# Kernel tuning notes

Measured on AMD Instinct MI355X. Metric: run time of the kernel, lower is better.

The kernel has to match this reference:

```python
import jax, jax.numpy as jnp
import numpy as np

NEG_SLOPE = 0.2
EPS = 1e-16

N_NODES = 50000
N_EDGES = 800000
IN_C = 256
HID_C = 64
HEADS = 4
OUT_C = 128
N_GRAPHS = 100


def setup_inputs() -> dict:
    key = jax.random.key(0)
    ks = jax.random.split(key, 12)
    x = jax.random.normal(ks[0], (N_NODES, IN_C), dtype=jnp.float32)
    edge_index = jax.random.randint(ks[1], (2, N_EDGES), 0, N_NODES, dtype=jnp.int64)
    batch = jnp.sort(jax.random.randint(ks[2], (N_NODES,), 0, N_GRAPHS, dtype=jnp.int64))
    s1 = 1.0 / np.sqrt(IN_C)
    s2 = 1.0 / np.sqrt(HEADS * HID_C)
    W1 = jax.random.uniform(ks[3], (IN_C, HEADS * HID_C), jnp.float32, -s1, s1)
    att_src1 = jax.random.uniform(ks[4], (HEADS, HID_C), jnp.float32, -s1, s1)
    att_dst1 = jax.random.uniform(ks[5], (HEADS, HID_C), jnp.float32, -s1, s1)
    bias1 = jnp.zeros((HEADS * HID_C,), jnp.float32)
    W2 = jax.random.uniform(ks[6], (HEADS * HID_C, OUT_C), jnp.float32, -s2, s2)
    att_src2 = jax.random.uniform(ks[7], (1, OUT_C), jnp.float32, -s2, s2)
    att_dst2 = jax.random.uniform(ks[8], (1, OUT_C), jnp.float32, -s2, s2)
    bias2 = jnp.zeros((OUT_C,), jnp.float32)
    return {"x": x, "W1": W1, "att_src1": att_src1, "att_dst1": att_dst1,
            "bias1": bias1, "W2": W2, "att_src2": att_src2, "att_dst2": att_dst2,
            "bias2": bias2, "edge_index": edge_index, "batch": batch,
            "num_graphs": N_GRAPHS}


def gat_conv(x, W, att_src, att_dst, bias, src, dst, heads, ch):
    # x: [N, F_in]; W: [F_in, heads*ch]; att_*: [heads, ch]
    n = x.shape[0]
    h = (x @ W).reshape(n, heads, ch)                      # [N, H, C]
    a_src = jnp.sum(h * att_src[None], axis=-1)            # [N, H]
    a_dst = jnp.sum(h * att_dst[None], axis=-1)            # [N, H]
    alpha = a_src[src] + a_dst[dst]                        # [E, H]
    alpha = jax.nn.leaky_relu(alpha, NEG_SLOPE)
    # segment softmax over destination nodes (every node has a self-loop)
    amax = jax.ops.segment_max(alpha, dst, num_segments=n)
    e = jnp.exp(alpha - amax[dst])
    denom = jax.ops.segment_sum(e, dst, num_segments=n)
    alpha = e / (denom[dst] + EPS)                         # [E, H]
    msg = h[src] * alpha[:, :, None]                       # [E, H, C]
    out = jax.ops.segment_sum(msg, dst, num_segments=n)    # [N, H, C]
    return out.reshape(n, heads * ch) + bias


def reference(x, W1, att_src1, att_dst1, bias1, W2, att_src2, att_dst2, bias2,
              edge_index, batch, num_graphs):
    n = x.shape[0]
    loops = jnp.arange(n, dtype=edge_index.dtype)
    src = jnp.concatenate([edge_index[0], loops])
    dst = jnp.concatenate([edge_index[1], loops])
    h = gat_conv(x, W1, att_src1, att_dst1, bias1, src, dst, HEADS, HID_C)
    h = jax.nn.relu(h)
    h = gat_conv(h, W2, att_src2, att_dst2, bias2, src, dst, 1, OUT_C)
    h = jax.nn.relu(h)
    # global mean pool over graphs
    sums = jax.ops.segment_sum(h, batch, num_segments=num_graphs)
    cnt = jax.ops.segment_sum(jnp.ones((n, 1), h.dtype), batch, num_segments=num_graphs)
    return sums / jnp.maximum(cnt, 1.0)
```

## Files before the change

kernel.cpp:

```cpp
#include <hip/hip_runtime.h>
#include <hip/hip_bf16.h>
#include <hip/hip_fp16.h>

#define N_NODES 50000
#define N_EDGES 800000
#define E_TOT   (N_EDGES + N_NODES)
#define IN_C    256
#define H1C     256
#define HEADS   4
#define HID_C   64
#define OUT_C   128
#define N_GRAPHS 100
#define NEG_SLOPE 0.2f
#define EPS_F 1e-16f

#define NBUCKET 391
#define BIN_BLOCKS 104
#define EDGES_PER_SB 8192
#define EBUF_CAP 4096
#define STAGE_CAP 4096
#define GEMM1_MB 391

#define PREP_BIN_BLOCKS    104
#define PREP_CAST_BLOCKS   12500
#define PREP_W1_BLOCKS     256
#define PREP_W2_BLOCKS     128
#define PREP_BOUNDS_BLOCKS 196
#define PREP_DOUT_BLOCKS   50
#define PREP_TOTAL (PREP_BIN_BLOCKS + PREP_CAST_BLOCKS + PREP_W1_BLOCKS + PREP_W2_BLOCKS + PREP_BOUNDS_BLOCKS + PREP_DOUT_BLOCKS)

typedef _Float16 half8_t __attribute__((ext_vector_type(8)));
typedef float f32x4 __attribute__((ext_vector_type(4)));

__device__ __forceinline__ void gll16(const void* g, void* l) {
    __builtin_amdgcn_global_load_lds(
        (const __attribute__((address_space(1))) void*)g,
        (__attribute__((address_space(3))) void*)l, 16, 0, 0);
}

__global__ __launch_bounds__(256) void prep_kernel(const float* __restrict__ x,
                                                   _Float16* __restrict__ xh,
                                                   const float* __restrict__ W1,
                                                   _Float16* __restrict__ W1t,
                                                   const float* __restrict__ W2,
                                                   _Float16* __restrict__ W2t,
                                                   const int* __restrict__ ei,
                                                   int* __restrict__ gcur,
                                                   int* __restrict__ ebuf,
                                                   const int* __restrict__ batch,
                                                   int* __restrict__ gstart,
                                                   float* __restrict__ d_out) {
    __shared__ int bh[NBUCKET];
    __shared__ int bofs[NBUCKET];
    int b = blockIdx.x;
    int tid = threadIdx.x;
    if (b < PREP_BIN_BLOCKS) {
        for (int t = tid; t < NBUCKET; t += 256) bh[t] = 0;
        __syncthreads();
        int base = b * EDGES_PER_SB;
#pragma unroll 4
        for (int k = 0; k < EDGES_PER_SB / 256; ++k) {
            int idx = base + k * 256 + tid;
            int d = -1;
            if (idx < N_EDGES) d = ei[N_EDGES + idx];
            else if (idx < E_TOT) d = idx - N_EDGES;
            if (d >= 0 && d < N_NODES) atomicAdd(&bh[d >> 7], 1);
        }
        __syncthreads();
        for (int t = tid; t < NBUCKET; t += 256) {
            int c = bh[t];
            bofs[t] = (c > 0) ? atomicAdd(&gcur[t], c) : 0;
            bh[t] = 0;
        }
        __syncthreads();
#pragma unroll 4
        for (int k = 0; k < EDGES_PER_SB / 256; ++k) {
            int idx = base + k * 256 + tid;
            int s = 0, d = -1;
            if (idx < N_EDGES) { s = ei[idx]; d = ei[N_EDGES + idx]; }
            else if (idx < E_TOT) { s = idx - N_EDGES; d = s; }
            if (d >= 0 && d < N_NODES) {
                int t = d >> 7;
                int p = bofs[t] + atomicAdd(&bh[t], 1);
                if (p < EBUF_CAP)
                    ebuf[t * EBUF_CAP + p] = (s & 0xFFFF) | ((d & 127) << 16);
            }
        }
        return;
    }
    b -= PREP_BIN_BLOCKS;
    if (b < PREP_CAST_BLOCKS) {
        int idx = b * 256 + tid;
        float4 v = reinterpret_cast<const float4*>(x)[idx];
        union { _Float16 h[4]; uint2 u; } p;
        p.h[0] = (_Float16)v.x; p.h[1] = (_Float16)v.y;
        p.h[2] = (_Float16)v.z; p.h[3] = (_Float16)v.w;
        reinterpret_cast<uint2*>(xh)[idx] = p.u;
        return;
    }
    b -= PREP_CAST_BLOCKS;
    if (b < PREP_W1_BLOCKS) {
        int idx = b * 256 + tid;
        int n = idx >> 8, k = idx & 255;
        W1t[idx] = (_Float16)W1[k * 256 + n];
        return;
    }
    b -= PREP_W1_BLOCKS;
    if (b < PREP_W2_BLOCKS) {
        int idx = b * 256 + tid;
        int n = idx >> 8, k = idx & 255;
        W2t[idx] = (_Float16)W2[k * 128 + n];
        return;
    }
    b -= PREP_W2_BLOCKS;
    if (b < PREP_BOUNDS_BLOCKS) {
        int idx = b * 256 + tid;
        if (idx >= N_NODES) return;
        int g = batch[idx];
        if (g < 0) g = 0; if (g >= N_GRAPHS) g = N_GRAPHS - 1;
        if (idx == 0) {
            for (int j = 0; j <= g; ++j) gstart[j] = 0;
        } else {
            int gp = batch[idx - 1];
            if (gp < 0) gp = 0; if (gp >= N_GRAPHS) gp = N_GRAPHS - 1;
            for (int j = gp + 1; j <= g; ++j) gstart[j] = idx;
        }
        if (idx == N_NODES - 1) {
            for (int j = g + 1; j <= N_GRAPHS; ++j) gstart[j] = N_NODES;
        }
        return;
    }
    b -= PREP_BOUNDS_BLOCKS;
    {
        int idx = b * 256 + tid;
        if (idx < N_GRAPHS * 128) d_out[idx] = 0.f;
    }
}

__global__ __launch_bounds__(256) void sort_gemm1_kernel(const int* __restrict__ gcur,
                                                         const int* __restrict__ ebuf,
                                                         int* __restrict__ ssrc,
                                                         int* __restrict__ row_ptr,
                                                         const _Float16* __restrict__ A,
                                                         const _Float16* __restrict__ Bt,
                                                         _Float16* __restrict__ C,
                                                         const float* __restrict__ attS,
                                                         const float* __restrict__ attD,
                                                         float* __restrict__ a_src_o,
                                                         float* __restrict__ a_dst_o) {
    __shared__ __align__(16) char smem[17408];
    __shared__ int s_off;
    const int tid = threadIdx.x;

    if (blockIdx.x < NBUCKET) {
        int* cnt   = reinterpret_cast<int*>(smem);
        int* sc    = cnt + 128;
        int* stage = sc + 128;
        int j = blockIdx.x;
        if (tid < 64) {
            int acc = 0;
            for (int i = tid; i < j; i += 64) {
                int c = gcur[i];
                acc += (c < EBUF_CAP) ? c : EBUF_CAP;
            }
#pragma unroll
            for (int off = 32; off > 0; off >>= 1) acc += __shfl_down(acc, off);
            if (tid == 0) s_off = acc;
        }
        if (tid < 128) cnt[tid] = 0;
        __syncthreads();
        int span = gcur[j]; if (span > EBUF_CAP) span = EBUF_CAP;
        int lo = s_off;
        const int* eb = ebuf + j * EBUF_CAP;
        for (int t = tid; t < span; t += 256)
            atomicAdd(&cnt[(eb[t] >> 16) & 127], 1);
        __syncthreads();
        if (tid < 128) sc[tid] = cnt[tid];
        __syncthreads();
#pragma unroll
        for (int off = 1; off < 128; off <<= 1) {
            int u = (tid >= off && tid < 128) ? sc[tid - off] : 0;
            __syncthreads();
            if (tid < 128) sc[tid] += u;
            __syncthreads();
        }
        int jn0 = j << 7;
        int nNodes = N_NODES - jn0; if (nNodes > 128) nNodes = 128;
        if (tid < 128) {
            int excl = sc[tid] - cnt[tid];
            if (tid < nNodes) row_ptr[jn0 + tid] = lo + excl;
            cnt[tid] = excl;
        }
        if (j == NBUCKET - 1 && tid == 0) row_ptr[N_NODES] = lo + span;
        __syncthreads();
        for (int t = tid; t < span; t += 256) {
            int v = eb[t];
            int p = atomicAdd(&cnt[(v >> 16) & 127], 1);
            stage[p] = v & 0xFFFF;
        }
        __syncthreads();
        for (int t = tid; t < span; t += 256) ssrc[lo + t] = stage[t];
        return;
    }

    _Float16* As = reinterpret_cast<_Float16*>(smem);
    _Float16* Bs = reinterpret_cast<_Float16*>(smem + 8192);
    int b2 = blockIdx.x - NBUCKET;
    const int tileM = (b2 >= GEMM1_MB ? b2 - GEMM1_MB : b2) * 128;
    const int tileN = (b2 >= GEMM1_MB) ? 128 : 0;
    const int w = tid >> 6, lane = tid & 63;
    const int wm = (w >> 1) * 64, wn = (w & 1) * 64;
    const int quad = lane >> 4, mlane = lane & 15;
    const int lrow = lane >> 2;
    const int pos  = lane & 3;
    const int ra0  = w * 16 + lrow;
    const int ra1  = ra0 + 64;
    const int ca0  = pos ^ ((ra0 >> 1) & 3);
    const int ca1  = pos ^ ((ra1 >> 1) & 3);

    f32x4 zero = {0.f, 0.f, 0.f, 0.f};
    f32x4 acc[4][4];
#pragma unroll
    for (int i = 0; i < 4; ++i)
#pragma unroll
        for (int j = 0; j < 4; ++j) acc[i][j] = zero;

    const _Float16* gA0 = A + (size_t)(tileM + ra0) * 256 + ca0 * 8;
    const _Float16* gA1 = A + (size_t)(tileM + ra1) * 256 + ca1 * 8;
    const _Float16* gB0 = Bt + (size_t)(tileN + ra0) * 256 + ca0 * 8;
    const _Float16* gB1 = Bt + (size_t)(tileN + ra1) * 256 + ca1 * 8;
    _Float16* lA0 = As + w * 512;
    _Float16* lA1 = As + 2048 + w * 512;
    _Float16* lB0 = Bs + w * 512;
    _Float16* lB1 = Bs + 2048 + w * 512;

    for (int k0 = 0; k0 < 256; k0 += 32) {
        __syncthreads();
        gll16(gA0 + k0, lA0);
        gll16(gA1 + k0, lA1);
        gll16(gB0 + k0, lB0);
        gll16(gB1 + k0, lB1);
        __syncthreads();
        half8_t af[4], bf[4];
#pragma unroll
        for (int mt = 0; mt < 4; ++mt) {
            int ra = wm + mt * 16 + mlane;
            af[mt] = *reinterpret_cast<const half8_t*>(As + ra * 32 + ((quad ^ ((ra >> 1) & 3)) << 3));
        }
#pragma unroll
        for (int nt = 0; nt < 4; ++nt) {
            int rb = wn + nt * 16 + mlane;
            bf[nt] = *reinterpret_cast<const half8_t*>(Bs + rb * 32 + ((quad ^ ((rb >> 1) & 3)) << 3));
        }
#pragma unroll
        for (int mt = 0; mt < 4; ++mt)
#pragma unroll
            for (int nt = 0; nt < 4; ++nt)
                acc[mt][nt] = __builtin_amdgcn_mfma_f32_16x16x32_f16(af[mt], bf[nt], acc[mt][nt], 0, 0, 0);
    }
#pragma unroll
    for (int mt = 0; mt < 4; ++mt) {
#pragma unroll
        for (int i = 0; i < 4; ++i) {
            int row = tileM + wm + mt * 16 + quad * 4 + i;
            if (row < N_NODES) {
                _Float16* cp = C + (size_t)row * 256 + tileN + wn;
#pragma unroll
                for (int nt = 0; nt < 4; ++nt)
                    cp[nt * 16 + mlane] = (_Float16)acc[mt][nt][i];
            }
        }
    }
    {
        int hd = (tileN + wn) >> 6;
        float as[4], ad[4];
#pragma unroll
        for (int nt = 0; nt < 4; ++nt) {
            as[nt] = attS[hd * 64 + nt * 16 + mlane];
            ad[nt] = attD[hd * 64 + nt * 16 + mlane];
        }
#pragma unroll
        for (int mt = 0; mt < 4; ++mt) {
#pragma unroll
            for (int i = 0; i < 4; ++i) {
                float ps = acc[mt][0][i] * as[0] + acc[mt][1][i] * as[1]
                         + acc[mt][2][i] * as[2] + acc[mt][3][i] * as[3];
                float pd = acc[mt][0][i] * ad[0] + acc[mt][1][i] * ad[1]
                         + acc[mt][2][i] * ad[2] + acc[mt][3][i] * ad[3];
#pragma unroll
                for (int off = 1; off < 16; off <<= 1) {
                    ps += __shfl_xor(ps, off);
                    pd += __shfl_xor(pd, off);
                }
                if (mlane == 0) {
                    int row = tileM + wm + mt * 16 + quad * 4 + i;
                    if (row < N_NODES) {
                        a_src_o[row * 4 + hd] = ps;
                        a_dst_o[row * 4 + hd] = pd;
                    }
                }
            }
        }
    }
}

__global__ __launch_bounds__(256) void gemm_mfma_kernel(const _Float16* __restrict__ A,
                                                        const _Float16* __restrict__ Bt,
                                                        _Float16* __restrict__ C,
                                                        const float* __restrict__ attS,
                                                        const float* __restrict__ attD,
                                                        float* __restrict__ a_src_o,
                                                        float* __restrict__ a_dst_o,
                                                        int M, int N) {
    __shared__ __align__(16) _Float16 As[4096];
    __shared__ __align__(16) _Float16 Bs[4096];
    __shared__ float lds_ps[128];
    __shared__ float lds_pd[128];
    const int tid = threadIdx.x;
    const int tileM = blockIdx.x * 128;
    const int tileN = 0;
    const int w = tid >> 6, lane = tid & 63;
    const int wm = (w >> 1) * 64, wn = (w & 1) * 64;
    const int quad = lane >> 4, mlane = lane & 15;
    const int lrow = lane >> 2;
    const int pos  = lane & 3;
    const int ra0  = w * 16 + lrow;
    const int ra1  = ra0 + 64;
    const int ca0  = pos ^ ((ra0 >> 1) & 3);
    const int ca1  = pos ^ ((ra1 >> 1) & 3);

    f32x4 zero = {0.f, 0.f, 0.f, 0.f};
    f32x4 acc[4][4];
#pragma unroll
    for (int i = 0; i < 4; ++i)
#pragma unroll
        for (int j = 0; j < 4; ++j) acc[i][j] = zero;

    const _Float16* gA0 = A + (size_t)(tileM + ra0) * 256 + ca0 * 8;
    const _Float16* gA1 = A + (size_t)(tileM + ra1) * 256 + ca1 * 8;
    const _Float16* gB0 = Bt + (size_t)(tileN + ra0) * 256 + ca0 * 8;
    const _Float16* gB1 = Bt + (size_t)(tileN + ra1) * 256 + ca1 * 8;
    _Float16* lA0 = As + w * 512;
    _Float16* lA1 = As + 2048 + w * 512;
    _Float16* lB0 = Bs + w * 512;
    _Float16* lB1 = Bs + 2048 + w * 512;

    for (int k0 = 0; k0 < 256; k0 += 32) {
        __syncthreads();
        gll16(gA0 + k0, lA0);
        gll16(gA1 + k0, lA1);
        gll16(gB0 + k0, lB0);
        gll16(gB1 + k0, lB1);
        __syncthreads();
        half8_t af[4], bf[4];
#pragma unroll
        for (int mt = 0; mt < 4; ++mt) {
            int ra = wm + mt * 16 + mlane;
            af[mt] = *reinterpret_cast<const half8_t*>(As + ra * 32 + ((quad ^ ((ra >> 1) & 3)) << 3));
        }
#pragma unroll
        for (int nt = 0; nt < 4; ++nt) {
            int rb = wn + nt * 16 + mlane;
            bf[nt] = *reinterpret_cast<const half8_t*>(Bs + rb * 32 + ((quad ^ ((rb >> 1) & 3)) << 3));
        }
#pragma unroll
        for (int mt = 0; mt < 4; ++mt)
#pragma unroll
            for (int nt = 0; nt < 4; ++nt)
                acc[mt][nt] = __builtin_amdgcn_mfma_f32_16x16x32_f16(af[mt], bf[nt], acc[mt][nt], 0, 0, 0);
    }
#pragma unroll
    for (int mt = 0; mt < 4; ++mt) {
#pragma unroll
        for (int i = 0; i < 4; ++i) {
            int row = tileM + wm + mt * 16 + quad * 4 + i;
            if (row < M) {
                _Float16* cp = C + (size_t)row * N + tileN + wn;
#pragma unroll
                for (int nt = 0; nt < 4; ++nt)
                    cp[nt * 16 + mlane] = (_Float16)acc[mt][nt][i];
            }
        }
    }
    {
        float as[4], ad[4];
#pragma unroll
        for (int nt = 0; nt < 4; ++nt) {
            as[nt] = attS[wn + nt * 16 + mlane];
            ad[nt] = attD[wn + nt * 16 + mlane];
        }
        float psa[4][4], pda[4][4];
#pragma unroll
        for (int mt = 0; mt < 4; ++mt) {
#pragma unroll
            for (int i = 0; i < 4; ++i) {
                float ps = acc[mt][0][i] * as[0] + acc[mt][1][i] * as[1]
                         + acc[mt][2][i] * as[2] + acc[mt][3][i] * as[3];
                float pd = acc[mt][0][i] * ad[0] + acc[mt][1][i] * ad[1]
                         + acc[mt][2][i] * ad[2] + acc[mt][3][i] * ad[3];
#pragma unroll
                for (int off = 1; off < 16; off <<= 1) {
                    ps += __shfl_xor(ps, off);
                    pd += __shfl_xor(pd, off);
                }
                psa[mt][i] = ps; pda[mt][i] = pd;
            }
        }
        __syncthreads();
        if (wn == 0 && mlane == 0) {
#pragma unroll
            for (int mt = 0; mt < 4; ++mt)
#pragma unroll
                for (int i = 0; i < 4; ++i) {
                    int lr = wm + mt * 16 + quad * 4 + i;
                    lds_ps[lr] = psa[mt][i];
                    lds_pd[lr] = pda[mt][i];
                }
        }
        __syncthreads();
        if (wn == 64 && mlane == 0) {
#pragma unroll
            for (int mt = 0; mt < 4; ++mt)
#pragma unroll
                for (int i = 0; i < 4; ++i) {
                    int lr = wm + mt * 16 + quad * 4 + i;
                    int row = tileM + lr;
                    if (row < M) {
                        a_src_o[row] = psa[mt][i] + lds_ps[lr];
                        a_dst_o[row] = pda[mt][i] + lds_pd[lr];
                    }
                }
        }
    }
}

__device__ __forceinline__ float lrelu(float x) { return x > 0.f ? x : NEG_SLOPE * x; }

__global__ __launch_bounds__(256) void edge1_kernel(const int* __restrict__ row_ptr,
                                                    const int* __restrict__ ssrc,
                                                    const __half* __restrict__ h1h,
                                                    const float* __restrict__ a_src,
                                                    const float* __restrict__ a_dst,
                                                    const float* __restrict__ bias,
                                                    __half* __restrict__ out) {
    int node = blockIdx.x * 4 + (threadIdx.x >> 6);
    int lane = threadIdx.x & 63;
    int hf   = lane >> 5;
    int cl   = lane & 31;
    int hd   = cl >> 3;
    int start = row_ptr[node], end = row_ptr[node + 1];
    int em1 = end - 1;
    float adh = a_dst[node * 4 + hd];

    const uint4* h1v = reinterpret_cast<const uint4*>(h1h);
    float4 aA0 = make_float4(0.f,0.f,0.f,0.f), aA1 = make_float4(0.f,0.f,0.f,0.f);
    float4 aB0 = make_float4(0.f,0.f,0.f,0.f), aB1 = make_float4(0.f,0.f,0.f,0.f);
    float s = 0.f;
    for (int e = start; e < end; e += 4) {
        int e0 = e + hf;
        int e1 = e + 2 + hf;
        int i0 = ssrc[e0 <= em1 ? e0 : em1];
        int i1 = ssrc[e1 <= em1 ? e1 : em1];
        float r0 = a_src[i0 * 4 + hd];
        float r1 = a_src[i1 * 4 + hd];
        uint4 q0 = h1v[(size_t)i0 * 32 + cl];
        uint4 q1 = h1v[(size_t)i1 * 32 + cl];
        float w0 = (e0 < end) ? __expf(lrelu(r0 + adh)) : 0.f;
        float w1 = (e1 < end) ? __expf(lrelu(r1 + adh)) : 0.f;
        s += w0 + w1;
        float2 f;
        f = __half22float2(*reinterpret_cast<const __half2*>(&q0.x)); aA0.x += w0*f.x; aA0.y += w0*f.y;
        f = __half22float2(*reinterpret_cast<const __half2*>(&q0.y)); aA0.z += w0*f.x; aA0.w += w0*f.y;
        f = __half22float2(*reinterpret_cast<const __half2*>(&q0.z)); aA1.x += w0*f.x; aA1.y += w0*f.y;
        f = __half22float2(*reinterpret_cast<const __half2*>(&q0.w)); aA1.z += w0*f.x; aA1.w += w0*f.y;
        f = __half22float2(*reinterpret_cast<const __half2*>(&q1.x)); aB0.x += w1*f.x; aB0.y += w1*f.y;
        f = __half22float2(*reinterpret_cast<const __half2*>(&q1.y)); aB0.z += w1*f.x; aB0.w += w1*f.y;
        f = __half22float2(*reinterpret_cast<const __half2*>(&q1.z)); aB1.x += w1*f.x; aB1.y += w1*f.y;
        f = __half22float2(*reinterpret_cast<const __half2*>(&q1.w)); aB1.z += w1*f.x; aB1.w += w1*f.y;
    }
    float4 c0, c1;
    c0.x = aA0.x + aB0.x; c0.y = aA0.y + aB0.y; c0.z = aA0.z + aB0.z; c0.w = aA0.w + aB0.w;
    c1.x = aA1.x + aB1.x; c1.y = aA1.y + aB1.y; c1.z = aA1.z + aB1.z; c1.w = aA1.w + aB1.w;
    c0.x += __shfl_xor(c0.x, 32); c0.y += __shfl_xor(c0.y, 32);
    c0.z += __shfl_xor(c0.z, 32); c0.w += __shfl_xor(c0.w, 32);
    c1.x += __shfl_xor(c1.x, 32); c1.y += __shfl_xor(c1.y, 32);
    c1.z += __shfl_xor(c1.z, 32); c1.w += __shfl_xor(c1.w, 32);
    s += __shfl_xor(s, 32);
    float inv = 1.0f / (s + EPS_F);
    if (lane < 32) {
        const float4* b4 = reinterpret_cast<const float4*>(bias);
        float4 b0 = b4[cl * 2], b1 = b4[cl * 2 + 1];
        union { _Float16 h[8]; uint4 u; } st;
        st.h[0] = (_Float16)fmaxf(c0.x * inv + b0.x, 0.f);
        st.h[1] = (_Float16)fmaxf(c0.y * inv + b0.y, 0.f);
        st.h[2] = (_Float16)fmaxf(c0.z * inv + b0.z, 0.f);
        st.h[3] = (_Float16)fmaxf(c0.w * inv + b0.w, 0.f);
        st.h[4] = (_Float16)fmaxf(c1.x * inv + b1.x, 0.f);
        st.h[5] = (_Float16)fmaxf(c1.y * inv + b1.y, 0.f);
        st.h[6] = (_Float16)fmaxf(c1.z * inv + b1.z, 0.f);
        st.h[7] = (_Float16)fmaxf(c1.w * inv + b1.w, 0.f);
        reinterpret_cast<uint4*>(out)[(size_t)node * 32 + cl] = st.u;
    }
}

__global__ __launch_bounds__(256) void edge2_kernel(const int* __restrict__ row_ptr,
                                                    const int* __restrict__ ssrc,
                                                    const __half* __restrict__ h2h,
                                                    const float* __restrict__ a_src,
                                                    const float* __restrict__ a_dst,
                                                    const float* __restrict__ bias,
                                                    float* __restrict__ out) {
    int lane = threadIdx.x & 63;
    int node = blockIdx.x * 8 + ((threadIdx.x >> 6) << 1) + (lane >> 5);
    int sub  = (lane >> 4) & 1;
    int cl   = lane & 15;
    int start = row_ptr[node], end = row_ptr[node + 1];
    int em1 = end - 1;
    float ad = a_dst[node];

    const uint4* h2v = reinterpret_cast<const uint4*>(h2h);
    float4 aA0 = make_float4(0.f,0.f,0.f,0.f), aA1 = make_float4(0.f,0.f,0.f,0.f);
    float4 aB0 = make_float4(0.f,0.f,0.f,0.f), aB1 = make_float4(0.f,0.f,0.f,0.f);
    float s = 0.f;
    for (int e = start; e < end; e += 4) {
        int e0 = e + sub;
        int e1 = e + 2 + sub;
        int i0 = ssrc[e0 <= em1 ? e0 : em1];
        int i1 = ssrc[e1 <= em1 ? e1 : em1];
        float r0 = a_src[i0];
        float r1 = a_src[i1];
        uint4 q0 = h2v[(size_t)i0 * 16 + cl];
        uint4 q1 = h2v[(size_t)i1 * 16 + cl];
        float w0 = (e0 < end) ? __expf(lrelu(r0 + ad)) : 0.f;
        float w1 = (e1 < end) ? __expf(lrelu(r1 + ad)) : 0.f;
        s += w0 + w1;
        float2 f;
        f = __half22float2(*reinterpret_cast<const __half2*>(&q0.x)); aA0.x += w0*f.x; aA0.y += w0*f.y;
        f = __half22float2(*reinterpret_cast<const __half2*>(&q0.y)); aA0.z += w0*f.x; aA0.w += w0*f.y;
        f = __half22float2(*reinterpret_cast<const __half2*>(&q0.z)); aA1.x += w0*f.x; aA1.y += w0*f.y;
        f = __half22float2(*reinterpret_cast<const __half2*>(&q0.w)); aA1.z += w0*f.x; aA1.w += w0*f.y;
        f = __half22float2(*reinterpret_cast<const __half2*>(&q1.x)); aB0.x += w1*f.x; aB0.y += w1*f.y;
        f = __half22float2(*reinterpret_cast<const __half2*>(&q1.y)); aB0.z += w1*f.x; aB0.w += w1*f.y;
        f = __half22float2(*reinterpret_cast<const __half2*>(&q1.z)); aB1.x += w1*f.x; aB1.y += w1*f.y;
        f = __half22float2(*reinterpret_cast<const __half2*>(&q1.w)); aB1.z += w1*f.x; aB1.w += w1*f.y;
    }
    float4 c0, c1;
    c0.x = aA0.x + aB0.x; c0.y = aA0.y + aB0.y; c0.z = aA0.z + aB0.z; c0.w = aA0.w + aB0.w;
    c1.x = aA1.x + aB1.x; c1.y = aA1.y + aB1.y; c1.z = aA1.z + aB1.z; c1.w = aA1.w + aB1.w;
    c0.x += __shfl_xor(c0.x, 16); c0.y += __shfl_xor(c0.y, 16);
    c0.z += __shfl_xor(c0.z, 16); c0.w += __shfl_xor(c0.w, 16);
    c1.x += __shfl_xor(c1.x, 16); c1.y += __shfl_xor(c1.y, 16);
    c1.z += __shfl_xor(c1.z, 16); c1.w += __shfl_xor(c1.w, 16);
    s += __shfl_xor(s, 16);
    float inv = 1.0f / (s + EPS_F);
    if (sub == 0) {
        const float4* b4 = reinterpret_cast<const float4*>(bias);
        float4 b0 = b4[cl * 2], b1 = b4[cl * 2 + 1];
        float4 o0, o1;
        o0.x = fmaxf(c0.x * inv + b0.x, 0.f);
        o0.y = fmaxf(c0.y * inv + b0.y, 0.f);
        o0.z = fmaxf(c0.z * inv + b0.z, 0.f);
        o0.w = fmaxf(c0.w * inv + b0.w, 0.f);
        o1.x = fmaxf(c1.x * inv + b1.x, 0.f);
        o1.y = fmaxf(c1.y * inv + b1.y, 0.f);
        o1.z = fmaxf(c1.z * inv + b1.z, 0.f);
        o1.w = fmaxf(c1.w * inv + b1.w, 0.f);
        float4* o4 = reinterpret_cast<float4*>(out) + (size_t)node * 32 + cl * 2;
        o4[0] = o0;
        o4[1] = o1;
    }
}

#define POOL_CHUNK 64
__global__ __launch_bounds__(128) void pool_kernel(const float* __restrict__ out2,
                                                   const int* __restrict__ batch,
                                                   const int* __restrict__ gstart,
                                                   float* __restrict__ d_out) {
    int c = threadIdx.x;
    int node0 = blockIdx.x * POOL_CHUNK;
    int nodeEnd = node0 + POOL_CHUNK; if (nodeEnd > N_NODES) nodeEnd = N_NODES;
    if (node0 >= N_NODES) return;
    int gprev = batch[node0];
    float acc = 0.f;
    for (int node = node0; node < nodeEnd; ++node) {
        int g = batch[node];
        if (g != gprev) {
            if (gprev >= 0 && gprev < N_GRAPHS) {
                float cnt = (float)(gstart[gprev + 1] - gstart[gprev]);
                if (cnt < 1.f) cnt = 1.f;
                atomicAdd(&d_out[gprev * 128 + c], acc / cnt);
            }
            acc = 0.f;
            gprev = g;
        }
        acc += out2[(size_t)node * 128 + c];
    }
    if (gprev >= 0 && gprev < N_GRAPHS) {
        float cnt = (float)(gstart[gprev + 1] - gstart[gprev]);
        if (cnt < 1.f) cnt = 1.f;
        atomicAdd(&d_out[gprev * 128 + c], acc / cnt);
    }
}

extern "C" void kernel_launch(void* const* d_in, const int* in_sizes, int n_in,
                              void* d_out_v, int out_size, void* d_ws, size_t ws_size,
                              hipStream_t stream) {
    const float* x      = (const float*)d_in[0];
    const float* W1     = (const float*)d_in[1];
    const float* att_s1 = (const float*)d_in[2];
    const float* att_d1 = (const float*)d_in[3];
    const float* bias1  = (const float*)d_in[4];
    const float* W2     = (const float*)d_in[5];
    const float* att_s2 = (const float*)d_in[6];
    const float* att_d2 = (const float*)d_in[7];
    const float* bias2  = (const float*)d_in[8];
    const int*   ei     = (const int*)d_in[9];
    const int*   batch  = (const int*)d_in[10];
    float* d_out = (float*)d_out_v;

    float* ws = (float*)d_ws;
    _Float16* xh    = (_Float16*)ws;
    _Float16* h1h   = (_Float16*)(ws + 6400000);
    _Float16* out1h = (_Float16*)(ws + 12800000);
    _Float16* h2h   = (_Float16*)ws;
    float*    out2  = ws + 6400000;
    float* a_src1 = ws + 19200000;
    float* a_dst1 = a_src1 + 200000;
    float* a_src2 = a_dst1 + 200000;
    float* a_dst2 = a_src2 + 50000;
    int* row_ptr  = (int*)(a_dst2 + 50000);
    int* ssrc     = row_ptr + 50016;
    int* ebuf     = ssrc + 850000;
    int* gcur     = ebuf + (NBUCKET * EBUF_CAP);
    int* gstart   = gcur + 512;
    _Float16* W1t = (_Float16*)(gstart + 128);
    _Float16* W2t = W1t + 65536;

    hipMemsetAsync(gcur, 0, 512 * sizeof(int), stream);

    prep_kernel<<<PREP_TOTAL, 256, 0, stream>>>(x, xh, W1, W1t, W2, W2t,
                                                ei, gcur, ebuf,
                                                batch, gstart, d_out);

    sort_gemm1_kernel<<<NBUCKET + GEMM1_MB * 2, 256, 0, stream>>>(
        gcur, ebuf, ssrc, row_ptr, xh, W1t, h1h,
        att_s1, att_d1, a_src1, a_dst1);

    edge1_kernel<<<N_NODES / 4, 256, 0, stream>>>(row_ptr, ssrc, (const __half*)h1h,
                                                  a_src1, a_dst1, bias1, (__half*)out1h);

    gemm_mfma_kernel<<<(N_NODES + 127) / 128, 256, 0, stream>>>(
        out1h, W2t, h2h, att_s2, att_d2, a_src2, a_dst2, N_NODES, OUT_C);

    edge2_kernel<<<N_NODES / 8, 256, 0, stream>>>(row_ptr, ssrc, (const __half*)h2h,
                                                  a_src2, a_dst2, bias2, out2);

    pool_kernel<<<(N_NODES + POOL_CHUNK - 1) / POOL_CHUNK, 128, 0, stream>>>(out2, batch, gstart, d_out);
}
```

Before: 293.3 us.

## Fuse fp32-to-fp16 cast of x into GEMM1 with full-width N tiles

Drops the separate prep pass that converts x to fp16 in a workspace buffer. GEMM1 now reads fp32 x directly, converts it in registers and writes it into shared memory. Each block is widened to 512 threads and covers all 256 output columns, so each A row is loaded once instead of twice. This removes a 51MB read plus 25MB write pass, at the cost of synchronous global loads for A instead of async LDS loads and larger blocks for the sort path.

```diff
diff --git a/kernel.cpp b/kernel.cpp
--- a/kernel.cpp
+++ b/kernel.cpp
@@ -15,19 +15,17 @@
 #define EPS_F 1e-16f
 
 #define NBUCKET 391
-#define BIN_BLOCKS 104
 #define EDGES_PER_SB 8192
 #define EBUF_CAP 4096
 #define STAGE_CAP 4096
 #define GEMM1_MB 391
 
 #define PREP_BIN_BLOCKS    104
-#define PREP_CAST_BLOCKS   12500
 #define PREP_W1_BLOCKS     256
 #define PREP_W2_BLOCKS     128
 #define PREP_BOUNDS_BLOCKS 196
 #define PREP_DOUT_BLOCKS   50
-#define PREP_TOTAL (PREP_BIN_BLOCKS + PREP_CAST_BLOCKS + PREP_W1_BLOCKS + PREP_W2_BLOCKS + PREP_BOUNDS_BLOCKS + PREP_DOUT_BLOCKS)
+#define PREP_TOTAL (PREP_BIN_BLOCKS + PREP_W1_BLOCKS + PREP_W2_BLOCKS + PREP_BOUNDS_BLOCKS + PREP_DOUT_BLOCKS)
 
 typedef _Float16 half8_t __attribute__((ext_vector_type(8)));
 typedef float f32x4 __attribute__((ext_vector_type(4)));
@@ -38,9 +36,7 @@
         (__attribute__((address_space(3))) void*)l, 16, 0, 0);
 }
 
-__global__ __launch_bounds__(256) void prep_kernel(const float* __restrict__ x,
-                                                   _Float16* __restrict__ xh,
-                                                   const float* __restrict__ W1,
+__global__ __launch_bounds__(256) void prep_kernel(const float* __restrict__ W1,
                                                    _Float16* __restrict__ W1t,
                                                    const float* __restrict__ W2,
                                                    _Float16* __restrict__ W2t,
@@ -89,16 +85,6 @@
         return;
     }
     b -= PREP_BIN_BLOCKS;
-    if (b < PREP_CAST_BLOCKS) {
-        int idx = b * 256 + tid;
-        float4 v = reinterpret_cast<const float4*>(x)[idx];
-        union { _Float16 h[4]; uint2 u; } p;
-        p.h[0] = (_Float16)v.x; p.h[1] = (_Float16)v.y;
-        p.h[2] = (_Float16)v.z; p.h[3] = (_Float16)v.w;
-        reinterpret_cast<uint2*>(xh)[idx] = p.u;
-        return;
-    }
-    b -= PREP_CAST_BLOCKS;
     if (b < PREP_W1_BLOCKS) {
         int idx = b * 256 + tid;
         int n = idx >> 8, k = idx & 255;
@@ -137,18 +123,18 @@
     }
 }
 
-__global__ __launch_bounds__(256) void sort_gemm1_kernel(const int* __restrict__ gcur,
+__global__ __launch_bounds__(512) void sort_gemm1_kernel(const int* __restrict__ gcur,
                                                          const int* __restrict__ ebuf,
                                                          int* __restrict__ ssrc,
                                                          int* __restrict__ row_ptr,
-                                                         const _Float16* __restrict__ A,
+                                                         const float* __restrict__ X,
                                                          const _Float16* __restrict__ Bt,
                                                          _Float16* __restrict__ C,
                                                          const float* __restrict__ attS,
                                                          const float* __restrict__ attD,
                                                          float* __restrict__ a_src_o,
                                                          float* __restrict__ a_dst_o) {
-    __shared__ __align__(16) char smem[17408];
+    __shared__ __align__(16) char smem[24576];
     __shared__ int s_off;
     const int tid = threadIdx.x;
 
@@ -172,7 +158,7 @@
         int span = gcur[j]; if (span > EBUF_CAP) span = EBUF_CAP;
         int lo = s_off;
         const int* eb = ebuf + j * EBUF_CAP;
-        for (int t = tid; t < span; t += 256)
+        for (int t = tid; t < span; t += 512)
             atomicAdd(&cnt[(eb[t] >> 16) & 127], 1);
         __syncthreads();
         if (tid < 128) sc[tid] = cnt[tid];
@@ -193,30 +179,34 @@
         }
         if (j == NBUCKET - 1 && tid == 0) row_ptr[N_NODES] = lo + span;
         __syncthreads();
-        for (int t = tid; t < span; t += 256) {
+        for (int t = tid; t < span; t += 512) {
             int v = eb[t];
             int p = atomicAdd(&cnt[(v >> 16) & 127], 1);
             stage[p] = v & 0xFFFF;
         }
         __syncthreads();
-        for (int t = tid; t < span; t += 256) ssrc[lo + t] = stage[t];
+        for (int t = tid; t < span; t += 512) ssrc[lo + t] = stage[t];
         return;
     }
 
     _Float16* As = reinterpret_cast<_Float16*>(smem);
     _Float16* Bs = reinterpret_cast<_Float16*>(smem + 8192);
-    int b2 = blockIdx.x - NBUCKET;
-    const int tileM = (b2 >= GEMM1_MB ? b2 - GEMM1_MB : b2) * 128;
-    const int tileN = (b2 >= GEMM1_MB) ? 128 : 0;
+    const int tileM = (blockIdx.x - NBUCKET) * 128;
     const int w = tid >> 6, lane = tid & 63;
-    const int wm = (w >> 1) * 64, wn = (w & 1) * 64;
+    const int wm = (w >> 2) * 64, wn = (w & 3) * 64;
     const int quad = lane >> 4, mlane = lane & 15;
-    const int lrow = lane >> 2;
-    const int pos  = lane & 3;
-    const int ra0  = w * 16 + lrow;
-    const int ra1  = ra0 + 64;
-    const int ca0  = pos ^ ((ra0 >> 1) & 3);
-    const int ca1  = pos ^ ((ra1 >> 1) & 3);
+    const int arow = tid >> 2;
+    const int apos = tid & 3;
+    const int ac   = apos ^ ((arow >> 1) & 3);
+    int axr = tileM + arow; if (axr > N_NODES - 1) axr = N_NODES - 1;
+    const float* gx = X + (size_t)axr * 256 + apos * 8;
+    const int lrow = lane >> 2, pos = lane & 3;
+    const int brow0 = w * 32 + lrow, brow1 = brow0 + 16;
+    const int bc0 = pos ^ ((brow0 >> 1) & 3), bc1 = pos ^ ((brow1 >> 1) & 3);
+    const _Float16* gB0 = Bt + (size_t)brow0 * 256 + bc0 * 8;
+    const _Float16* gB1 = Bt + (size_t)brow1 * 256 + bc1 * 8;
+    _Float16* lB0 = Bs + w * 1024;
+    _Float16* lB1 = Bs + w * 1024 + 512;
 
     f32x4 zero = {0.f, 0.f, 0.f, 0.f};
     f32x4 acc[4][4];
@@ -225,21 +215,18 @@
 #pragma unroll
         for (int j = 0; j < 4; ++j) acc[i][j] = zero;
 
-    const _Float16* gA0 = A + (size_t)(tileM + ra0) * 256 + ca0 * 8;
-    const _Float16* gA1 = A + (size_t)(tileM + ra1) * 256 + ca1 * 8;
-    const _Float16* gB0 = Bt + (size_t)(tileN + ra0) * 256 + ca0 * 8;
-    const _Float16* gB1 = Bt + (size_t)(tileN + ra1) * 256 + ca1 * 8;
-    _Float16* lA0 = As + w * 512;
-    _Float16* lA1 = As + 2048 + w * 512;
-    _Float16* lB0 = Bs + w * 512;
-    _Float16* lB1 = Bs + 2048 + w * 512;
-
     for (int k0 = 0; k0 < 256; k0 += 32) {
         __syncthreads();
-        gll16(gA0 + k0, lA0);
-        gll16(gA1 + k0, lA1);
         gll16(gB0 + k0, lB0);
         gll16(gB1 + k0, lB1);
+        float4 va = *reinterpret_cast<const float4*>(gx + k0);
+        float4 vb = *reinterpret_cast<const float4*>(gx + k0 + 4);
+        union { _Float16 h[8]; uint4 u; } pk;
+        pk.h[0] = (_Float16)va.x; pk.h[1] = (_Float16)va.y;
+        pk.h[2] = (_Float16)va.z; pk.h[3] = (_Float16)va.w;
+        pk.h[4] = (_Float16)vb.x; pk.h[5] = (_Float16)vb.y;
+        pk.h[6] = (_Float16)vb.z; pk.h[7] = (_Float16)vb.w;
+        *reinterpret_cast<uint4*>(As + arow * 32 + ac * 8) = pk.u;
         __syncthreads();
         half8_t af[4], bf[4];
 #pragma unroll
@@ -264,7 +251,7 @@
         for (int i = 0; i < 4; ++i) {
             int row = tileM + wm + mt * 16 + quad * 4 + i;
             if (row < N_NODES) {
-                _Float16* cp = C + (size_t)row * 256 + tileN + wn;
+                _Float16* cp = C + (size_t)row * 256 + wn;
 #pragma unroll
                 for (int nt = 0; nt < 4; ++nt)
                     cp[nt * 16 + mlane] = (_Float16)acc[mt][nt][i];
@@ -272,7 +259,7 @@
         }
     }
     {
-        int hd = (tileN + wn) >> 6;
+        int hd = w & 3;
         float as[4], ad[4];
 #pragma unroll
         for (int nt = 0; nt < 4; ++nt) {
@@ -619,7 +606,6 @@
     float* d_out = (float*)d_out_v;
 
     float* ws = (float*)d_ws;
-    _Float16* xh    = (_Float16*)ws;
     _Float16* h1h   = (_Float16*)(ws + 6400000);
     _Float16* out1h = (_Float16*)(ws + 12800000);
     _Float16* h2h   = (_Float16*)ws;
@@ -638,12 +624,12 @@
 
     hipMemsetAsync(gcur, 0, 512 * sizeof(int), stream);
 
-    prep_kernel<<<PREP_TOTAL, 256, 0, stream>>>(x, xh, W1, W1t, W2, W2t,
+    prep_kernel<<<PREP_TOTAL, 256, 0, stream>>>(W1, W1t, W2, W2t,
                                                 ei, gcur, ebuf,
                                                 batch, gstart, d_out);
 
-    sort_gemm1_kernel<<<NBUCKET + GEMM1_MB * 2, 256, 0, stream>>>(
-        gcur, ebuf, ssrc, row_ptr, xh, W1t, h1h,
+    sort_gemm1_kernel<<<NBUCKET + GEMM1_MB, 512, 0, stream>>>(
+        gcur, ebuf, ssrc, row_ptr, x, W1t, h1h,
         att_s1, att_d1, a_src1, a_dst1);
 
     edge1_kernel<<<N_NODES / 4, 256, 0, stream>>>(row_ptr, ssrc, (const __half*)h1h,
```

New measurement: 289.8 us. Within noise of the previous version (-1.2%).
